# Performance work log

Hardware: AMD Instinct MI355X
Metric: run time of the kernel (lower is better)

Reference implementation:

```python
import jax, jax.numpy as jnp
import numpy as np
from jax import lax

B, N, S, K = 16, 8192, 1024, 32
FACTOR = 1.0
EPS_BN = 1e-5


def farthest_point_sample(xyz, npoint):
    # xyz: [B, N, 3] -> idx [B, npoint]. Deterministic start at index 0
    # (torch version starts at a random index; start choice doesn't change the math pattern).
    b, n, _ = xyz.shape
    bidx = jnp.arange(b)

    def step(carry, _):
        distance, farthest = carry
        centroid = xyz[bidx, farthest]                      # [B, 3]
        dist = jnp.sum((xyz - centroid[:, None, :]) ** 2, -1)  # [B, N]
        distance = jnp.minimum(distance, dist)
        new_far = jnp.argmax(distance, axis=-1)
        return (distance, new_far), farthest

    init = (jnp.full((b, n), 1e10, xyz.dtype), jnp.zeros((b,), jnp.int32))
    _, idxs = lax.scan(step, init, None, length=npoint)
    return idxs.T  # [B, npoint]


def square_distance(src, dst):
    # [B,Ns,3] x [B,Nd,3] -> [B,Ns,Nd]
    d = -2.0 * jnp.einsum('bnc,bmc->bnm', src, dst)
    d += jnp.sum(src ** 2, -1)[:, :, None]
    d += jnp.sum(dst ** 2, -1)[:, None, :]
    return d


def safe_cdist(x):
    # x: [B, C, S]; pairwise euclidean over rows -> [B, C, C]; zero-safe sqrt
    diff = x[:, :, None, :] - x[:, None, :, :]          # [B, C, C, S]
    sq = jnp.sum(diff * diff, -1)
    pos = sq > 0
    return jnp.where(pos, jnp.sqrt(jnp.where(pos, sq, 1.0)), 0.0)


def batchnorm(x, gamma, beta, axes):
    mean = jnp.mean(x, axes, keepdims=True)
    var = jnp.var(x, axes, keepdims=True)  # biased, as in torch BN normalization
    return (x - mean) / jnp.sqrt(var + EPS_BN) * gamma + beta


def reference(xyz, bn1_gamma, bn1_beta, bn2_gamma, bn2_beta):
    b = xyz.shape[0]
    # --- FPS sampling ---
    fps_idx = farthest_point_sample(lax.stop_gradient(xyz), S)          # [B,S]
    new_xyz = jnp.take_along_axis(xyz, fps_idx[:, :, None], axis=1)     # [B,S,3]
    # --- kNN grouping ---
    sq = square_distance(lax.stop_gradient(new_xyz), lax.stop_gradient(xyz))  # [B,S,N]
    _, knn_idx = lax.top_k(-sq, K)                                      # [B,S,K] indices
    grouped = jax.vmap(lambda p, i: p[i])(xyz, knn_idx)                 # [B,S,K,3]
    diff = grouped - new_xyz[:, :, None, :]
    std = jnp.std(diff, ddof=1)                                         # scalar, unbiased like torch.std
    knn_norm = diff / (std + 1e-5)
    center = jnp.broadcast_to(new_xyz[:, :, None, :], (b, S, K, 3))
    knn_xyz = jnp.concatenate([knn_norm, center], axis=-1)              # [B,S,K,6]
    # --- Pooling over neighbors ---
    x = jnp.transpose(knn_xyz, (0, 3, 1, 2))                            # [B,6,S,K]
    lc = jnp.max(x, -1) + jnp.mean(x, -1)                               # [B,6,S]
    lc = jax.nn.relu(batchnorm(lc, bn1_gamma[None, :, None], bn1_beta[None, :, None], (0, 2)))
    # --- Consecutive representation (cdist + superdiagonal factor) ---
    tfcw = safe_cdist(lc)                                               # [B,6,6]
    i = jnp.arange(5)
    tfcw = tfcw.at[:, i, i + 1].multiply(FACTOR)
    # --- Pooling2 ---
    feat = tfcw.reshape(b, -1)                                          # [B,36]
    feat = jax.nn.relu(batchnorm(feat, bn2_gamma[None, :], bn2_beta[None, :], (0,)))
    return feat


def setup_inputs() -> dict:
    key = jax.random.key(0)
    k1, = jax.random.split(key, 1)
    return {
        'xyz': jax.random.normal(k1, (B, N, 3), dtype=jnp.float32),
        'bn1_gamma': jnp.ones((6,), jnp.float32),
        'bn1_beta': jnp.zeros((6,), jnp.float32),
        'bn2_gamma': jnp.ones((36,), jnp.float32),
        'bn2_beta': jnp.zeros((36,), jnp.float32),
    }
```

## Files before the change

### kernel.cpp

```cpp
#include <hip/hip_runtime.h>
#include <hip/hip_bf16.h>

constexpr int BB = 16;
constexpr int NN = 8192;
constexpr int SS = 1024;
constexpr int KK = 32;
constexpr int BUFC = 256;

__device__ __forceinline__ float b2f(__hip_bfloat16 h) { return __bfloat162float(h); }

__device__ __forceinline__ unsigned mkey32(float d) {
    unsigned u = __float_as_uint(d);
    return u ^ (0x80000000u | (unsigned)((int)u >> 31));
}

__device__ __forceinline__ unsigned long long dist_key(const float* __restrict__ pb,
                                                       int idx, float qx, float qy,
                                                       float qz, float qq) {
    float px = pb[idx * 3 + 0];
    float py = pb[idx * 3 + 1];
    float pz = pb[idx * 3 + 2];
    float dot = __fadd_rn(__fadd_rn(__fmul_rn(qx, px), __fmul_rn(qy, py)), __fmul_rn(qz, pz));
    float pp  = __fadd_rn(__fadd_rn(__fmul_rn(px, px), __fmul_rn(py, py)), __fmul_rn(pz, pz));
    float d = __fadd_rn(__fadd_rn(__fmul_rn(-2.0f, dot), qq), pp);
    return ((unsigned long long)mkey32(d) << 32) | (unsigned)idx;
}

template <int CTRL, int RMASK>
__device__ __forceinline__ unsigned long long dppmove_u64(unsigned long long v) {
    int lo = (int)(unsigned)v, hi = (int)(unsigned)(v >> 32);
    int nlo = __builtin_amdgcn_update_dpp(lo, lo, CTRL, RMASK, 0xf, false);
    int nhi = __builtin_amdgcn_update_dpp(hi, hi, CTRL, RMASK, 0xf, false);
    return ((unsigned long long)(unsigned)nhi << 32) | (unsigned)nlo;
}

template <int CTRL, int RMASK>
__device__ __forceinline__ double dppmax_f64(double v) {
    double m = __longlong_as_double(
        dppmove_u64<CTRL, RMASK>((unsigned long long)__double_as_longlong(v)));
    return fmax(v, m);
}

__device__ __forceinline__ double wave_max_dpp_f64(double v) {
    v = dppmax_f64<0x121, 0xf>(v);
    v = dppmax_f64<0x122, 0xf>(v);
    v = dppmax_f64<0x124, 0xf>(v);
    v = dppmax_f64<0x128, 0xf>(v);
    v = dppmax_f64<0x142, 0xa>(v);
    v = dppmax_f64<0x143, 0xc>(v);
    return v;
}

__device__ __forceinline__ unsigned long long bitonic64(unsigned long long v, int lane) {
#pragma unroll
    for (int k = 2; k <= 64; k <<= 1) {
#pragma unroll
        for (int j = k >> 1; j > 0; j >>= 1) {
            unsigned long long p = __shfl_xor(v, j);
            bool up = ((lane & k) == 0);
            bool lower = ((lane & j) == 0);
            bool take_min = (up == lower);
            v = take_min ? (p < v ? p : v) : (p > v ? p : v);
        }
    }
    return v;
}

__device__ __forceinline__ unsigned expand3(unsigned v) {
    v &= 0x3FFu;
    v = (v | (v << 16)) & 0x030000FFu;
    v = (v | (v << 8))  & 0x0300F00Fu;
    v = (v | (v << 4))  & 0x030C30C3u;
    v = (v | (v << 2))  & 0x09249249u;
    return v;
}

__global__ __launch_bounds__(256) void convert_kernel(
    const void* __restrict__ xyz_raw, const void* __restrict__ g1r,
    const void* __restrict__ b1r, const void* __restrict__ g2r,
    const void* __restrict__ b2r, float* __restrict__ xyzf,
    float* __restrict__ params, void* __restrict__ out_raw) {
    const unsigned short* u = (const unsigned short*)xyz_raw;
    unsigned short s = u[2 * (threadIdx.x & 63)];
    int e = (s >> 7) & 0xFF;
    unsigned long long m = __ballot(e >= 100 && e <= 140);
    bool isbf = __popcll(m) > 48;

    const int NT = BB * NN * 3;
    int tid = blockIdx.x * blockDim.x + threadIdx.x;
    int stride = gridDim.x * blockDim.x;
    if (isbf) {
        const __hip_bfloat16* p = (const __hip_bfloat16*)xyz_raw;
        for (int i = tid; i < NT; i += stride) xyzf[i] = b2f(p[i]);
    } else {
        const float* p = (const float*)xyz_raw;
        for (int i = tid; i < NT; i += stride) xyzf[i] = p[i];
    }
    if (blockIdx.x == 0 && threadIdx.x < 85) {
        int t = threadIdx.x;
        if (t == 84) {
            params[84] = isbf ? 1.0f : 0.0f;
        } else {
            const void* src; int off;
            if (t < 6)       { src = g1r; off = t; }
            else if (t < 12) { src = b1r; off = t - 6; }
            else if (t < 48) { src = g2r; off = t - 12; }
            else             { src = b2r; off = t - 48; }
            params[t] = isbf ? b2f(((const __hip_bfloat16*)src)[off])
                             : ((const float*)src)[off];
        }
    }
    if (blockIdx.x == 1 && threadIdx.x < 64) {
        for (int i = threadIdx.x; i < 576; i += 64) {
            if (isbf) ((__hip_bfloat16*)out_raw)[i] = __float2bfloat16(1.0f);
            else      ((float*)out_raw)[i] = 1.0f;
        }
    }
}

__global__ __attribute__((amdgpu_flat_work_group_size(512, 512)))
__attribute__((amdgpu_waves_per_eu(2, 2)))
void fps_kernel(const float* __restrict__ xyzf, float* __restrict__ new_xyz) {
    constexpr int T = 512, P = NN / T;
    const int b = blockIdx.x, t = threadIdx.x;
    const float* xb = xyzf + (size_t)b * NN * 3;

    __shared__ float sxyz[NN * 3];
    __shared__ unsigned sortk[NN];
    __shared__ double skey[2][8];
    __shared__ float sred[6][8];
    __shared__ float sbb[6];

    for (int i = t; i < NN * 3; i += T) sxyz[i] = xb[i];
    __syncthreads();

    {
        float mn[3] = {3.4e38f, 3.4e38f, 3.4e38f};
        float mx[3] = {-3.4e38f, -3.4e38f, -3.4e38f};
        for (int j = 0; j < P; j++) {
            int p = t + j * T;
#pragma unroll
            for (int c = 0; c < 3; c++) {
                float v = sxyz[p * 3 + c];
                mn[c] = fminf(mn[c], v);
                mx[c] = fmaxf(mx[c], v);
            }
        }
#pragma unroll
        for (int o = 32; o > 0; o >>= 1) {
#pragma unroll
            for (int c = 0; c < 3; c++) {
                mn[c] = fminf(mn[c], __shfl_xor(mn[c], o));
                mx[c] = fmaxf(mx[c], __shfl_xor(mx[c], o));
            }
        }
        int wv = t >> 6, ln = t & 63;
        if (ln == 0) {
#pragma unroll
            for (int c = 0; c < 3; c++) { sred[c][wv] = mn[c]; sred[3 + c][wv] = mx[c]; }
        }
        __syncthreads();
        if (t < 6) {
            bool ismin = t < 3;
            float v = sred[t][0];
            for (int w = 1; w < 8; w++) v = ismin ? fminf(v, sred[t][w]) : fmaxf(v, sred[t][w]);
            sbb[t] = v;
        }
        __syncthreads();
    }

    {
        float bx = sbb[0], by = sbb[1], bz = sbb[2];
        float qsx = 63.0f / fmaxf(sbb[3] - bx, 1e-9f);
        float qsy = 63.0f / fmaxf(sbb[4] - by, 1e-9f);
        float qsz = 63.0f / fmaxf(sbb[5] - bz, 1e-9f);
        for (int p = t; p < NN; p += T) {
            unsigned qx = (unsigned)min(63, (int)((sxyz[p * 3 + 0] - bx) * qsx));
            unsigned qy = (unsigned)min(63, (int)((sxyz[p * 3 + 1] - by) * qsy));
            unsigned qz = (unsigned)min(63, (int)((sxyz[p * 3 + 2] - bz) * qsz));
            unsigned m = (expand3(qx) << 2) | (expand3(qy) << 1) | expand3(qz);
            sortk[p] = (m << 13) | (unsigned)p;
        }
        __syncthreads();
        for (unsigned k = 2; k <= (unsigned)NN; k <<= 1) {
            for (unsigned j = k >> 1; j > 0; j >>= 1) {
#pragma unroll
                for (int r = 0; r < NN / 2 / T; r++) {
                    unsigned gid = (unsigned)(r * T + t);
                    unsigned i = ((gid & ~(j - 1)) << 1) | (gid & (j - 1));
                    unsigned p2 = i | j;
                    unsigned a = sortk[i], c2 = sortk[p2];
                    bool up = ((i & k) == 0);
                    if ((a > c2) == up) { sortk[i] = c2; sortk[p2] = a; }
                }
                __syncthreads();
            }
        }
    }

    float px[P], py[P], pz[P], ds[P];
    int nidx[P];
    float lox = 3.4e38f, loy = 3.4e38f, loz = 3.4e38f;
    float hix = -3.4e38f, hiy = -3.4e38f, hiz = -3.4e38f;
#pragma unroll
    for (int j = 0; j < P; j++) {
        unsigned oi = sortk[t * P + j] & 8191u;
        float x = sxyz[oi * 3 + 0];
        float y = sxyz[oi * 3 + 1];
        float z = sxyz[oi * 3 + 2];
        px[j] = x; py[j] = y; pz[j] = z;
        ds[j] = 1e10f;
        nidx[j] = (int)~oi;
        lox = fminf(lox, x); hix = fmaxf(hix, x);
        loy = fminf(loy, y); hiy = fmaxf(hiy, y);
        loz = fminf(loz, z); hiz = fmaxf(hiz, z);
    }
    __syncthreads();
    float* samples = (float*)sortk;

    float cx = xb[0], cy = xb[1], cz = xb[2];
    if (t == 0) { samples[0] = cx; samples[1] = cy; samples[2] = cz; }
    const int wave = t >> 6, lane = t & 63;

    double bk = 0.0;
    float tb = 1e10f;

    for (int step = 1; step < SS; step++) {
        float ax = fmaxf(fmaxf(__fsub_rn(lox, cx), __fsub_rn(cx, hix)), 0.0f);
        float ay = fmaxf(fmaxf(__fsub_rn(loy, cy), __fsub_rn(cy, hiy)), 0.0f);
        float az = fmaxf(fmaxf(__fsub_rn(loz, cz), __fsub_rn(cz, hiz)), 0.0f);
        float lbd = ax * ax + ay * ay + az * az;
        if (lbd * 0.999f < tb) {
            double kk[P];
#pragma unroll
            for (int j = 0; j < P; j++) {
                float dx = __fsub_rn(px[j], cx);
                float dy = __fsub_rn(py[j], cy);
                float dz = __fsub_rn(pz[j], cz);
                float d = __fadd_rn(__fadd_rn(__fmul_rn(dx, dx), __fmul_rn(dy, dy)),
                                    __fmul_rn(dz, dz));
                float mm = fminf(ds[j], d);
                ds[j] = mm;
                kk[j] = __hiloint2double(__float_as_int(mm), nidx[j]);
            }
#pragma unroll
            for (int w2 = P / 2; w2 > 0; w2 >>= 1)
#pragma unroll
                for (int j = 0; j < w2; j++) kk[j] = fmax(kk[j], kk[j + w2]);
            bk = kk[0];
            tb = __uint_as_float((unsigned)__double2hiint(bk));
        }

        double wk = wave_max_dpp_f64(bk);
        const int par = step & 1;
        if (lane == 63) skey[par][wave] = wk;
        __syncthreads();

        double k0 = fmax(skey[par][0], skey[par][1]);
        double k1 = fmax(skey[par][2], skey[par][3]);
        double k2 = fmax(skey[par][4], skey[par][5]);
        double k3 = fmax(skey[par][6], skey[par][7]);
        double bkk = fmax(fmax(k0, k1), fmax(k2, k3));

        unsigned gidx = ~(unsigned)(unsigned long long)__double_as_longlong(bkk);
        cx = sxyz[gidx * 3 + 0];
        cy = sxyz[gidx * 3 + 1];
        cz = sxyz[gidx * 3 + 2];
        if (t == 0) {
            samples[step * 3 + 0] = cx;
            samples[step * 3 + 1] = cy;
            samples[step * 3 + 2] = cz;
        }
    }

    __syncthreads();
    float* o = new_xyz + (size_t)b * SS * 3;
    for (int i = t; i < SS * 3; i += T) o[i] = samples[i];
}

__global__ __launch_bounds__(256, 2) void knn_kernel(const float* __restrict__ xyzf,
                                                     const float* __restrict__ new_xyz,
                                                     float* __restrict__ A,
                                                     double* __restrict__ qstats) {
    __shared__ unsigned long long buf[4][BUFC];
    const int t = threadIdx.x;
    const int lane = t & 63, wv = t >> 6;
    const int w = blockIdx.x * 4 + wv;
    const int b = w >> 10, s = w & 1023;

    const float* q = new_xyz + ((size_t)b * SS + s) * 3;
    float qx = q[0], qy = q[1], qz = q[2];
    float qq = __fadd_rn(__fadd_rn(__fmul_rn(qx, qx), __fmul_rn(qy, qy)), __fmul_rn(qz, qz));

    const float* pb = xyzf + (size_t)b * NN * 3;
    const unsigned long long ltmask = (1ull << lane) - 1ull;

    unsigned long long lmin = ~0ull;
    for (int j = 0; j < 128; j++) {
        unsigned long long key = dist_key(pb, j * 64 + lane, qx, qy, qz, qq);
        lmin = key < lmin ? key : lmin;
    }

    unsigned long long vs = bitonic64(lmin, lane);
    unsigned long long That = __shfl(vs, 31);

    for (int i = lane; i < BUFC; i += 64) buf[wv][i] = ~0ull;
    int base = 0;
    for (int j = 0; j < 128; j++) {
        unsigned long long key = dist_key(pb, j * 64 + lane, qx, qy, qz, qq);
        bool f = key <= That;
        unsigned long long bal = __ballot(f);
        int pos = base + __popcll(bal & ltmask);
        if (f && pos < BUFC) buf[wv][pos] = key;
        base += __popcll(bal);
    }

    if (base > BUFC) {
        unsigned lo = 0, hi = (unsigned)(That >> 32);
        for (int it = 0; it < 32; it++) {
            unsigned mid = lo + ((hi - lo) >> 1);
            int c = 0;
            for (int j = 0; j < 128; j++) {
                unsigned long long key = dist_key(pb, j * 64 + lane, qx, qy, qz, qq);
                c += ((unsigned)(key >> 32) <= mid) ? 1 : 0;
            }
#pragma unroll
            for (int o = 32; o > 0; o >>= 1) c += __shfl_xor(c, o);
            if (c >= 32) hi = mid; else lo = mid + 1;
        }
        That = ((unsigned long long)hi << 32) | 0xFFFFFFFFull;
        for (int i = lane; i < BUFC; i += 64) buf[wv][i] = ~0ull;
        base = 0;
        for (int j = 0; j < 128; j++) {
            unsigned long long key = dist_key(pb, j * 64 + lane, qx, qy, qz, qq);
            bool f = key <= That;
            unsigned long long bal = __ballot(f);
            int pos = base + __popcll(bal & ltmask);
            if (f && pos < BUFC) buf[wv][pos] = key;
            base += __popcll(bal);
        }
        if (base > BUFC) base = BUFC;
    }

    int M = base;
    unsigned long long kept = ~0ull;
    if (M <= 64) {
        unsigned long long v = (lane < M) ? buf[wv][lane] : ~0ull;
        v = bitonic64(v, lane);
        kept = v;
    } else {
        unsigned long long c0 = buf[wv][lane];
        unsigned long long c1 = buf[wv][64 + lane];
        unsigned long long c2 = buf[wv][128 + lane];
        unsigned long long c3 = buf[wv][192 + lane];
        for (int r = 0; r < KK; r++) {
            unsigned long long m01 = c0 < c1 ? c0 : c1;
            unsigned long long m23 = c2 < c3 ? c2 : c3;
            unsigned long long mm = m01 < m23 ? m01 : m23;
#pragma unroll
            for (int o = 32; o > 0; o >>= 1) {
                unsigned long long t2 = __shfl_xor(mm, o);
                mm = t2 < mm ? t2 : mm;
            }
            if (lane == r) kept = mm;
            c0 = (c0 == mm) ? ~0ull : c0;
            c1 = (c1 == mm) ? ~0ull : c1;
            c2 = (c2 == mm) ? ~0ull : c2;
            c3 = (c3 == mm) ? ~0ull : c3;
        }
    }

    bool act = (lane < KK);
    float gx = 0.0f, gy = 0.0f, gz = 0.0f;
    if (act) {
        unsigned nidx = (unsigned)kept;
        gx = pb[nidx * 3 + 0];
        gy = pb[nidx * 3 + 1];
        gz = pb[nidx * 3 + 2];
    }
    float dx = __fsub_rn(gx, qx);
    float dy = __fsub_rn(gy, qy);
    float dz = __fsub_rn(gz, qz);
    float mx = act ? dx : -3.402823466e38f;
    float my = act ? dy : -3.402823466e38f;
    float mz = act ? dz : -3.402823466e38f;
    float sx = act ? dx : 0.0f;
    float sy = act ? dy : 0.0f;
    float sz = act ? dz : 0.0f;
    double s1 = act ? ((double)dx + (double)dy + (double)dz) : 0.0;
    double s2 = act ? ((double)dx * dx + (double)dy * dy + (double)dz * dz) : 0.0;
#pragma unroll
    for (int o = 32; o > 0; o >>= 1) {
        mx = fmaxf(mx, __shfl_xor(mx, o));
        my = fmaxf(my, __shfl_xor(my, o));
        mz = fmaxf(mz, __shfl_xor(mz, o));
        sx += __shfl_xor(sx, o);
        sy += __shfl_xor(sy, o);
        sz += __shfl_xor(sz, o);
        s1 += __shfl_xor(s1, o);
        s2 += __shfl_xor(s2, o);
    }
    if (lane == 0) {
        float* a = A + ((size_t)b * SS + s) * 3;
        a[0] = __fadd_rn(mx, __fmul_rn(sx, 0.03125f));
        a[1] = __fadd_rn(my, __fmul_rn(sy, 0.03125f));
        a[2] = __fadd_rn(mz, __fmul_rn(sz, 0.03125f));
        qstats[2 * w + 0] = s1;
        qstats[2 * w + 1] = s2;
    }
}

__global__ __launch_bounds__(256) void reduce_stats_kernel(const double* __restrict__ qstats,
                                                           double* __restrict__ stats) {
    __shared__ double r1[4], r2[4];
    int t = threadIdx.x;
    double a = 0.0, bsum = 0.0;
    for (int i = t; i < BB * SS; i += 256) { a += qstats[2 * i]; bsum += qstats[2 * i + 1]; }
#pragma unroll
    for (int o = 32; o > 0; o >>= 1) { a += __shfl_xor(a, o); bsum += __shfl_xor(bsum, o); }
    int wv = t >> 6, ln = t & 63;
    if (ln == 0) { r1[wv] = a; r2[wv] = bsum; }
    __syncthreads();
    if (t == 0) {
        stats[0] = r1[0] + r1[1] + r1[2] + r1[3];
        stats[1] = r2[0] + r2[1] + r2[2] + r2[3];
    }
}

__global__ __launch_bounds__(256) void lc_kernel(const float* __restrict__ new_xyz,
                                                 const float* __restrict__ A,
                                                 const double* __restrict__ stats,
                                                 float* __restrict__ lc,
                                                 double* __restrict__ bn1acc) {
    __shared__ double red[4];
    const int b = blockIdx.x / 6, c = blockIdx.x % 6;
    const int t = threadIdx.x;
    const double n = (double)BB * SS * KK * 3;
    double sd = stats[0], sq = stats[1];
    double var = (sq - sd * sd / n) / (n - 1.0);
    float stdv = (float)sqrt(var);
    float denom = __fadd_rn(stdv, 1e-5f);

    double s1 = 0.0, s2 = 0.0;
    for (int r = 0; r < 4; r++) {
        int s = r * 256 + t;
        float v;
        if (c < 3) {
            v = A[((size_t)b * SS + s) * 3 + c] / denom;
        } else {
            float ww = new_xyz[((size_t)b * SS + s) * 3 + (c - 3)];
            v = __fadd_rn(ww, ww);
        }
        lc[((size_t)b * 6 + c) * SS + s] = v;
        s1 += (double)v;
        s2 += (double)v * (double)v;
    }
#pragma unroll
    for (int off = 32; off > 0; off >>= 1) { s1 += __shfl_down(s1, off); s2 += __shfl_down(s2, off); }
    int wv = t >> 6, ln = t & 63;
    if (ln == 0) red[wv] = s1;
    __syncthreads();
    if (t == 0) atomicAdd(&bn1acc[c * 2 + 0], red[0] + red[1] + red[2] + red[3]);
    __syncthreads();
    if (ln == 0) red[wv] = s2;
    __syncthreads();
    if (t == 0) atomicAdd(&bn1acc[c * 2 + 1], red[0] + red[1] + red[2] + red[3]);
}

__global__ __launch_bounds__(256) void cdist_kernel(const float* __restrict__ lc,
                                                    const double* __restrict__ bn1acc,
                                                    const float* __restrict__ params,
                                                    float* __restrict__ tf) {
    __shared__ float sy[6 * SS];
    const int b = blockIdx.x, t = threadIdx.x;
    float mean[6], sde[6], gg[6], bt[6];
    const double n = (double)BB * SS;
#pragma unroll
    for (int c = 0; c < 6; c++) {
        double m = bn1acc[c * 2 + 0] / n;
        double v = bn1acc[c * 2 + 1] / n - m * m;
        mean[c] = (float)m;
        sde[c] = sqrtf((float)v + 1e-5f);
        gg[c] = params[c];
        bt[c] = params[6 + c];
    }
    for (int r = 0; r < 24; r++) {
        int g = r * 256 + t;
        int c = g >> 10;
        float v = lc[(size_t)b * 6 * SS + g];
        float y = (v - mean[c]) / sde[c] * gg[c] + bt[c];
        sy[g] = fmaxf(y, 0.0f);
    }
    __syncthreads();
    if (t < 6) tf[b * 36 + t * 7] = 0.0f;

    const int w = t >> 6, lane = t & 63;
    const int PI[15] = {0,0,0,0,0,1,1,1,1,2,2,2,3,3,4};
    const int PJ[15] = {1,2,3,4,5,2,3,4,5,3,4,5,4,5,5};
    for (int r = 0; r < 4; r++) {
        int p = w + r * 4;
        if (p < 15) {
            int i = PI[p], j = PJ[p];
            float acc = 0.0f;
            for (int m2 = 0; m2 < 16; m2++) {
                int s = lane + m2 * 64;
                float d = sy[i * SS + s] - sy[j * SS + s];
                acc += d * d;
            }
#pragma unroll
            for (int off = 32; off > 0; off >>= 1) acc += __shfl_down(acc, off);
            if (lane == 0) {
                float v = acc > 0.0f ? sqrtf(acc) : 0.0f;
                const float FACTOR = 1.0f;
                tf[b * 36 + i * 6 + j] = (j == i + 1) ? v * FACTOR : v;
                tf[b * 36 + j * 6 + i] = v;
            }
        }
    }
}

__global__ __launch_bounds__(64) void bn2_kernel(const float* __restrict__ tf,
                                                 const float* __restrict__ params,
                                                 void* __restrict__ out_raw) {
    int f = threadIdx.x;
    if (f >= 36) return;
    bool isbf = params[84] != 0.0f;
    float x[16]; float sum = 0.0f;
#pragma unroll
    for (int b = 0; b < 16; b++) { x[b] = tf[b * 36 + f]; sum += x[b]; }
    float mean = sum * 0.0625f;
    float vs = 0.0f;
#pragma unroll
    for (int b = 0; b < 16; b++) { float d = x[b] - mean; vs += d * d; }
    float var = vs * 0.0625f;
    float denom = sqrtf(var + 1e-5f);
    float g = params[12 + f], bb = params[48 + f];
#pragma unroll
    for (int b = 0; b < 16; b++) {
        float y = (x[b] - mean) / denom * g + bb;
        y = fmaxf(y, 0.0f);
        if (isbf) ((__hip_bfloat16*)out_raw)[b * 36 + f] = __float2bfloat16(y);
        else      ((float*)out_raw)[b * 36 + f] = y;
    }
}

extern "C" void kernel_launch(void* const* d_in, const int* in_sizes, int n_in,
                              void* d_out, int out_size, void* d_ws, size_t ws_size,
                              hipStream_t stream) {
    const void* xyz_raw = d_in[0];
    const void* g1r = d_in[1]; const void* b1r = d_in[2];
    const void* g2r = d_in[3]; const void* b2r = d_in[4];
    {
        const void* six[2] = {nullptr, nullptr}; int n6 = 0;
        const void* t36[2] = {nullptr, nullptr}; int n36 = 0;
        const void* big = nullptr;
        for (int i = 0; i < n_in; i++) {
            if (in_sizes[i] == BB * NN * 3) big = d_in[i];
            else if (in_sizes[i] == 6  && n6  < 2) six[n6++]  = d_in[i];
            else if (in_sizes[i] == 36 && n36 < 2) t36[n36++] = d_in[i];
        }
        if (big && n6 == 2 && n36 == 2) {
            xyz_raw = big; g1r = six[0]; b1r = six[1]; g2r = t36[0]; b2r = t36[1];
        }
    }

    char* ws = (char*)d_ws;
    float* xyzf    = (float*)(ws + 0);
    float* new_xyz = (float*)(ws + 1572864);
    float* A       = (float*)(ws + 1769472);
    float* lc      = (float*)(ws + 1966080);
    float* tf      = (float*)(ws + 2359296);
    double* stats  = (double*)(ws + 2361600);
    double* bn1acc = stats + 2;
    float* params  = (float*)(ws + 2361712);
    double* qstats = (double*)(ws + 2362112);

    hipMemsetAsync(stats, 0, 14 * sizeof(double), stream);
    hipLaunchKernelGGL(convert_kernel, dim3(512), dim3(256), 0, stream,
                       xyz_raw, g1r, b1r, g2r, b2r, xyzf, params, d_out);
    hipLaunchKernelGGL(fps_kernel,          dim3(16),   dim3(512), 0, stream, xyzf, new_xyz);
    hipLaunchKernelGGL(knn_kernel,          dim3(4096), dim3(256), 0, stream, xyzf, new_xyz, A, qstats);
    hipLaunchKernelGGL(reduce_stats_kernel, dim3(1),    dim3(256), 0, stream, qstats, stats);
    hipLaunchKernelGGL(lc_kernel,           dim3(96),   dim3(256), 0, stream, new_xyz, A, stats, lc, bn1acc);
    hipLaunchKernelGGL(cdist_kernel,        dim3(16),   dim3(256), 0, stream, lc, bn1acc, params, tf);
    hipLaunchKernelGGL(bn2_kernel,          dim3(1),    dim3(64),  0, stream, tf, params, d_out);

    (void)in_sizes; (void)n_in; (void)out_size; (void)ws_size;
}
```

Measured before the change: 1.155 ms.

## Process two batches per FPS block and carry winner coordinates through reduction

The FPS kernel now handles two batch elements per 512-thread block (8 blocks instead of 16). The two independent serial chains are interleaved within each step so their latencies overlap and share one barrier per step. The shared-memory copy of the point cloud is dropped; each wave picks out its winning point's coordinates from registers and publishes them alongside the key, so the cross-wave reduction yields the centroid directly. The wave reduction is now an all-lanes max using shuffles. In exchange, per-thread register pressure roughly doubles, which may cause spills, and only 8 CUs are used for this serial kernel.

```diff
diff --git a/kernel.cpp b/kernel.cpp
--- a/kernel.cpp
+++ b/kernel.cpp
@@ -41,13 +41,13 @@
     return fmax(v, m);
 }
 
-__device__ __forceinline__ double wave_max_dpp_f64(double v) {
+__device__ __forceinline__ double wave_allmax_f64(double v) {
     v = dppmax_f64<0x121, 0xf>(v);
     v = dppmax_f64<0x122, 0xf>(v);
     v = dppmax_f64<0x124, 0xf>(v);
     v = dppmax_f64<0x128, 0xf>(v);
-    v = dppmax_f64<0x142, 0xa>(v);
-    v = dppmax_f64<0x143, 0xc>(v);
+    v = fmax(v, __shfl_xor(v, 16));
+    v = fmax(v, __shfl_xor(v, 32));
     return v;
 }
 
@@ -73,6 +73,15 @@
     v = (v | (v << 4))  & 0x030C30C3u;
     v = (v | (v << 2))  & 0x09249249u;
     return v;
+}
+
+__device__ __forceinline__ void sel2(double& k, float& x, float& y, float& z,
+                                     double kb, float xb, float yb, float zb) {
+    bool g = kb > k;
+    k = g ? kb : k;
+    x = g ? xb : x;
+    y = g ? yb : y;
+    z = g ? zb : z;
 }
 
 __global__ __launch_bounds__(256) void convert_kernel(
@@ -123,159 +132,244 @@
 void fps_kernel(const float* __restrict__ xyzf, float* __restrict__ new_xyz) {
     constexpr int T = 512, P = NN / T;
     const int b = blockIdx.x, t = threadIdx.x;
-    const float* xb = xyzf + (size_t)b * NN * 3;
-
-    __shared__ float sxyz[NN * 3];
+    const float* xbA = xyzf + (size_t)(2 * b) * NN * 3;
+    const float* xbB = xyzf + (size_t)(2 * b + 1) * NN * 3;
+
     __shared__ unsigned sortk[NN];
-    __shared__ double skey[2][8];
+    __shared__ double skeyL[2][2][8];
+    __shared__ float4 scoordL[2][2][8];
     __shared__ float sred[6][8];
     __shared__ float sbb[6];
 
-    for (int i = t; i < NN * 3; i += T) sxyz[i] = xb[i];
+    const int wave = t >> 6, lane = t & 63;
+
+    float pxA[P], pyA[P], pzA[P], dsA[P]; unsigned uniA[P / 2];
+    float loxA, loyA, lozA, hixA, hiyA, hizA, cxA, cyA, czA;
+    float pxB[P], pyB[P], pzB[P], dsB[P]; unsigned uniB[P / 2];
+    float loxB, loyB, lozB, hixB, hiyB, hizB, cxB, cyB, czB;
+
+    auto setup = [&](const float* __restrict__ xb, float (&px)[P], float (&py)[P],
+                     float (&pz)[P], float (&ds)[P], unsigned (&uni)[P / 2],
+                     float& lox, float& loy, float& loz,
+                     float& hix, float& hiy, float& hiz,
+                     float& cx, float& cy, float& cz) {
+        {
+            float mn[3] = {3.4e38f, 3.4e38f, 3.4e38f};
+            float mx[3] = {-3.4e38f, -3.4e38f, -3.4e38f};
+            for (int j = 0; j < P; j++) {
+                int p = t + j * T;
+#pragma unroll
+                for (int c = 0; c < 3; c++) {
+                    float v = xb[p * 3 + c];
+                    mn[c] = fminf(mn[c], v);
+                    mx[c] = fmaxf(mx[c], v);
+                }
+            }
+#pragma unroll
+            for (int o = 32; o > 0; o >>= 1) {
+#pragma unroll
+                for (int c = 0; c < 3; c++) {
+                    mn[c] = fminf(mn[c], __shfl_xor(mn[c], o));
+                    mx[c] = fmaxf(mx[c], __shfl_xor(mx[c], o));
+                }
+            }
+            if (lane == 0) {
+#pragma unroll
+                for (int c = 0; c < 3; c++) { sred[c][wave] = mn[c]; sred[3 + c][wave] = mx[c]; }
+            }
+            __syncthreads();
+            if (t < 6) {
+                bool ismin = t < 3;
+                float v = sred[t][0];
+                for (int w = 1; w < 8; w++) v = ismin ? fminf(v, sred[t][w]) : fmaxf(v, sred[t][w]);
+                sbb[t] = v;
+            }
+            __syncthreads();
+        }
+        {
+            float bx = sbb[0], by = sbb[1], bz = sbb[2];
+            float qsx = 63.0f / fmaxf(sbb[3] - bx, 1e-9f);
+            float qsy = 63.0f / fmaxf(sbb[4] - by, 1e-9f);
+            float qsz = 63.0f / fmaxf(sbb[5] - bz, 1e-9f);
+            for (int p = t; p < NN; p += T) {
+                unsigned qx = (unsigned)min(63, (int)((xb[p * 3 + 0] - bx) * qsx));
+                unsigned qy = (unsigned)min(63, (int)((xb[p * 3 + 1] - by) * qsy));
+                unsigned qz = (unsigned)min(63, (int)((xb[p * 3 + 2] - bz) * qsz));
+                unsigned m = (expand3(qx) << 2) | (expand3(qy) << 1) | expand3(qz);
+                sortk[p] = (m << 13) | (unsigned)p;
+            }
+            __syncthreads();
+            for (unsigned k = 2; k <= (unsigned)NN; k <<= 1) {
+                for (unsigned j = k >> 1; j > 0; j >>= 1) {
+#pragma unroll
+                    for (int r = 0; r < NN / 2 / T; r++) {
+                        unsigned gid = (unsigned)(r * T + t);
+                        unsigned i = ((gid & ~(j - 1)) << 1) | (gid & (j - 1));
+                        unsigned p2 = i | j;
+                        unsigned a = sortk[i], c2 = sortk[p2];
+                        bool up = ((i & k) == 0);
+                        if ((a > c2) == up) { sortk[i] = c2; sortk[p2] = a; }
+                    }
+                    __syncthreads();
+                }
+            }
+        }
+        lox = 3.4e38f; loy = 3.4e38f; loz = 3.4e38f;
+        hix = -3.4e38f; hiy = -3.4e38f; hiz = -3.4e38f;
+#pragma unroll
+        for (int j = 0; j < P; j++) {
+            unsigned oi = sortk[t * P + j] & 8191u;
+            float x = xb[oi * 3 + 0];
+            float y = xb[oi * 3 + 1];
+            float z = xb[oi * 3 + 2];
+            px[j] = x; py[j] = y; pz[j] = z;
+            ds[j] = 1e10f;
+            if ((j & 1) == 0) uni[j >> 1] = oi; else uni[j >> 1] |= (oi << 16);
+            lox = fminf(lox, x); hix = fmaxf(hix, x);
+            loy = fminf(loy, y); hiy = fmaxf(hiy, y);
+            loz = fminf(loz, z); hiz = fmaxf(hiz, z);
+        }
+        cx = xb[0]; cy = xb[1]; cz = xb[2];
+        __syncthreads();
+    };
+
+    setup(xbA, pxA, pyA, pzA, dsA, uniA, loxA, loyA, lozA, hixA, hiyA, hizA, cxA, cyA, czA);
+    setup(xbB, pxB, pyB, pzB, dsB, uniB, loxB, loyB, lozB, hixB, hiyB, hizB, cxB, cyB, czB);
+
+    float* samplesA = (float*)sortk;
+    float* samplesB = samplesA + SS * 3;
+
+    if (t == 0) {
+        samplesA[0] = cxA; samplesA[1] = cyA; samplesA[2] = czA;
+        samplesB[0] = cxB; samplesB[1] = cyB; samplesB[2] = czB;
+    }
+
+    double bkA = 0.0, bkB = 0.0;
+    float tbA = 1e10f, tbB = 1e10f;
+
+    for (int step = 1; step < SS; step++) {
+        const int par = step & 1;
+
+        {
+            float ax = fmaxf(fmaxf(__fsub_rn(loxA, cxA), __fsub_rn(cxA, hixA)), 0.0f);
+            float ay = fmaxf(fmaxf(__fsub_rn(loyA, cyA), __fsub_rn(cyA, hiyA)), 0.0f);
+            float az = fmaxf(fmaxf(__fsub_rn(lozA, czA), __fsub_rn(czA, hizA)), 0.0f);
+            float lbd = ax * ax + ay * ay + az * az;
+            if (lbd * 0.999f < tbA) {
+                double kk[P];
+#pragma unroll
+                for (int j = 0; j < P; j++) {
+                    float dx = __fsub_rn(pxA[j], cxA);
+                    float dy = __fsub_rn(pyA[j], cyA);
+                    float dz = __fsub_rn(pzA[j], czA);
+                    float d = __fadd_rn(__fadd_rn(__fmul_rn(dx, dx), __fmul_rn(dy, dy)),
+                                        __fmul_rn(dz, dz));
+                    float mm = fminf(dsA[j], d);
+                    dsA[j] = mm;
+                    unsigned oi = (uniA[j >> 1] >> ((j & 1) * 16)) & 0xFFFFu;
+                    kk[j] = __hiloint2double(__float_as_int(mm), (int)~oi);
+                }
+#pragma unroll
+                for (int w2 = P / 2; w2 > 0; w2 >>= 1)
+#pragma unroll
+                    for (int j = 0; j < w2; j++) kk[j] = fmax(kk[j], kk[j + w2]);
+                bkA = kk[0];
+                tbA = __uint_as_float((unsigned)__double2hiint(bkA));
+            }
+            double wk = wave_allmax_f64(bkA);
+            if (bkA == wk) {
+                unsigned widx = ~(unsigned)(unsigned long long)__double_as_longlong(bkA);
+                float wx = pxA[0], wy = pyA[0], wz = pzA[0];
+#pragma unroll
+                for (int j = 1; j < P; j++) {
+                    unsigned oi = (uniA[j >> 1] >> ((j & 1) * 16)) & 0xFFFFu;
+                    bool m = (oi == widx);
+                    wx = m ? pxA[j] : wx; wy = m ? pyA[j] : wy; wz = m ? pzA[j] : wz;
+                }
+                skeyL[0][par][wave] = bkA;
+                scoordL[0][par][wave] = make_float4(wx, wy, wz, 0.0f);
+            }
+        }
+        {
+            float ax = fmaxf(fmaxf(__fsub_rn(loxB, cxB), __fsub_rn(cxB, hixB)), 0.0f);
+            float ay = fmaxf(fmaxf(__fsub_rn(loyB, cyB), __fsub_rn(cyB, hiyB)), 0.0f);
+            float az = fmaxf(fmaxf(__fsub_rn(lozB, czB), __fsub_rn(czB, hizB)), 0.0f);
+            float lbd = ax * ax + ay * ay + az * az;
+            if (lbd * 0.999f < tbB) {
+                double kk[P];
+#pragma unroll
+                for (int j = 0; j < P; j++) {
+                    float dx = __fsub_rn(pxB[j], cxB);
+                    float dy = __fsub_rn(pyB[j], cyB);
+                    float dz = __fsub_rn(pzB[j], czB);
+                    float d = __fadd_rn(__fadd_rn(__fmul_rn(dx, dx), __fmul_rn(dy, dy)),
+                                        __fmul_rn(dz, dz));
+                    float mm = fminf(dsB[j], d);
+                    dsB[j] = mm;
+                    unsigned oi = (uniB[j >> 1] >> ((j & 1) * 16)) & 0xFFFFu;
+                    kk[j] = __hiloint2double(__float_as_int(mm), (int)~oi);
+                }
+#pragma unroll
+                for (int w2 = P / 2; w2 > 0; w2 >>= 1)
+#pragma unroll
+                    for (int j = 0; j < w2; j++) kk[j] = fmax(kk[j], kk[j + w2]);
+                bkB = kk[0];
+                tbB = __uint_as_float((unsigned)__double2hiint(bkB));
+            }
+            double wk = wave_allmax_f64(bkB);
+            if (bkB == wk) {
+                unsigned widx = ~(unsigned)(unsigned long long)__double_as_longlong(bkB);
+                float wx = pxB[0], wy = pyB[0], wz = pzB[0];
+#pragma unroll
+                for (int j = 1; j < P; j++) {
+                    unsigned oi = (uniB[j >> 1] >> ((j & 1) * 16)) & 0xFFFFu;
+                    bool m = (oi == widx);
+                    wx = m ? pxB[j] : wx; wy = m ? pyB[j] : wy; wz = m ? pzB[j] : wz;
+                }
+                skeyL[1][par][wave] = bkB;
+                scoordL[1][par][wave] = make_float4(wx, wy, wz, 0.0f);
+            }
+        }
+
+        __syncthreads();
+
+        {
+            double K0 = skeyL[0][par][0], K1 = skeyL[0][par][1], K2 = skeyL[0][par][2], K3 = skeyL[0][par][3];
+            double K4 = skeyL[0][par][4], K5 = skeyL[0][par][5], K6 = skeyL[0][par][6], K7 = skeyL[0][par][7];
+            float4 C0 = scoordL[0][par][0], C1 = scoordL[0][par][1], C2 = scoordL[0][par][2], C3 = scoordL[0][par][3];
+            float4 C4 = scoordL[0][par][4], C5 = scoordL[0][par][5], C6 = scoordL[0][par][6], C7 = scoordL[0][par][7];
+            sel2(K0, C0.x, C0.y, C0.z, K1, C1.x, C1.y, C1.z);
+            sel2(K2, C2.x, C2.y, C2.z, K3, C3.x, C3.y, C3.z);
+            sel2(K4, C4.x, C4.y, C4.z, K5, C5.x, C5.y, C5.z);
+            sel2(K6, C6.x, C6.y, C6.z, K7, C7.x, C7.y, C7.z);
+            sel2(K0, C0.x, C0.y, C0.z, K2, C2.x, C2.y, C2.z);
+            sel2(K4, C4.x, C4.y, C4.z, K6, C6.x, C6.y, C6.z);
+            sel2(K0, C0.x, C0.y, C0.z, K4, C4.x, C4.y, C4.z);
+            cxA = C0.x; cyA = C0.y; czA = C0.z;
+        }
+        {
+            double K0 = skeyL[1][par][0], K1 = skeyL[1][par][1], K2 = skeyL[1][par][2], K3 = skeyL[1][par][3];
+            double K4 = skeyL[1][par][4], K5 = skeyL[1][par][5], K6 = skeyL[1][par][6], K7 = skeyL[1][par][7];
+            float4 C0 = scoordL[1][par][0], C1 = scoordL[1][par][1], C2 = scoordL[1][par][2], C3 = scoordL[1][par][3];
+            float4 C4 = scoordL[1][par][4], C5 = scoordL[1][par][5], C6 = scoordL[1][par][6], C7 = scoordL[1][par][7];
+            sel2(K0, C0.x, C0.y, C0.z, K1, C1.x, C1.y, C1.z);
+            sel2(K2, C2.x, C2.y, C2.z, K3, C3.x, C3.y, C3.z);
+            sel2(K4, C4.x, C4.y, C4.z, K5, C5.x, C5.y, C5.z);
+            sel2(K6, C6.x, C6.y, C6.z, K7, C7.x, C7.y, C7.z);
+            sel2(K0, C0.x, C0.y, C0.z, K2, C2.x, C2.y, C2.z);
+            sel2(K4, C4.x, C4.y, C4.z, K6, C6.x, C6.y, C6.z);
+            sel2(K0, C0.x, C0.y, C0.z, K4, C4.x, C4.y, C4.z);
+            cxB = C0.x; cyB = C0.y; czB = C0.z;
+        }
+        if (t == 0) {
+            samplesA[step * 3 + 0] = cxA; samplesA[step * 3 + 1] = cyA; samplesA[step * 3 + 2] = czA;
+            samplesB[step * 3 + 0] = cxB; samplesB[step * 3 + 1] = cyB; samplesB[step * 3 + 2] = czB;
+        }
+    }
+
     __syncthreads();
-
-    {
-        float mn[3] = {3.4e38f, 3.4e38f, 3.4e38f};
-        float mx[3] = {-3.4e38f, -3.4e38f, -3.4e38f};
-        for (int j = 0; j < P; j++) {
-            int p = t + j * T;
-#pragma unroll
-            for (int c = 0; c < 3; c++) {
-                float v = sxyz[p * 3 + c];
-                mn[c] = fminf(mn[c], v);
-                mx[c] = fmaxf(mx[c], v);
-            }
-        }
-#pragma unroll
-        for (int o = 32; o > 0; o >>= 1) {
-#pragma unroll
-            for (int c = 0; c < 3; c++) {
-                mn[c] = fminf(mn[c], __shfl_xor(mn[c], o));
-                mx[c] = fmaxf(mx[c], __shfl_xor(mx[c], o));
-            }
-        }
-        int wv = t >> 6, ln = t & 63;
-        if (ln == 0) {
-#pragma unroll
-            for (int c = 0; c < 3; c++) { sred[c][wv] = mn[c]; sred[3 + c][wv] = mx[c]; }
-        }
-        __syncthreads();
-        if (t < 6) {
-            bool ismin = t < 3;
-            float v = sred[t][0];
-            for (int w = 1; w < 8; w++) v = ismin ? fminf(v, sred[t][w]) : fmaxf(v, sred[t][w]);
-            sbb[t] = v;
-        }
-        __syncthreads();
-    }
-
-    {
-        float bx = sbb[0], by = sbb[1], bz = sbb[2];
-        float qsx = 63.0f / fmaxf(sbb[3] - bx, 1e-9f);
-        float qsy = 63.0f / fmaxf(sbb[4] - by, 1e-9f);
-        float qsz = 63.0f / fmaxf(sbb[5] - bz, 1e-9f);
-        for (int p = t; p < NN; p += T) {
-            unsigned qx = (unsigned)min(63, (int)((sxyz[p * 3 + 0] - bx) * qsx));
-            unsigned qy = (unsigned)min(63, (int)((sxyz[p * 3 + 1] - by) * qsy));
-            unsigned qz = (unsigned)min(63, (int)((sxyz[p * 3 + 2] - bz) * qsz));
-            unsigned m = (expand3(qx) << 2) | (expand3(qy) << 1) | expand3(qz);
-            sortk[p] = (m << 13) | (unsigned)p;
-        }
-        __syncthreads();
-        for (unsigned k = 2; k <= (unsigned)NN; k <<= 1) {
-            for (unsigned j = k >> 1; j > 0; j >>= 1) {
-#pragma unroll
-                for (int r = 0; r < NN / 2 / T; r++) {
-                    unsigned gid = (unsigned)(r * T + t);
-                    unsigned i = ((gid & ~(j - 1)) << 1) | (gid & (j - 1));
-                    unsigned p2 = i | j;
-                    unsigned a = sortk[i], c2 = sortk[p2];
-                    bool up = ((i & k) == 0);
-                    if ((a > c2) == up) { sortk[i] = c2; sortk[p2] = a; }
-                }
-                __syncthreads();
-            }
-        }
-    }
-
-    float px[P], py[P], pz[P], ds[P];
-    int nidx[P];
-    float lox = 3.4e38f, loy = 3.4e38f, loz = 3.4e38f;
-    float hix = -3.4e38f, hiy = -3.4e38f, hiz = -3.4e38f;
-#pragma unroll
-    for (int j = 0; j < P; j++) {
-        unsigned oi = sortk[t * P + j] & 8191u;
-        float x = sxyz[oi * 3 + 0];
-        float y = sxyz[oi * 3 + 1];
-        float z = sxyz[oi * 3 + 2];
-        px[j] = x; py[j] = y; pz[j] = z;
-        ds[j] = 1e10f;
-        nidx[j] = (int)~oi;
-        lox = fminf(lox, x); hix = fmaxf(hix, x);
-        loy = fminf(loy, y); hiy = fmaxf(hiy, y);
-        loz = fminf(loz, z); hiz = fmaxf(hiz, z);
-    }
-    __syncthreads();
-    float* samples = (float*)sortk;
-
-    float cx = xb[0], cy = xb[1], cz = xb[2];
-    if (t == 0) { samples[0] = cx; samples[1] = cy; samples[2] = cz; }
-    const int wave = t >> 6, lane = t & 63;
-
-    double bk = 0.0;
-    float tb = 1e10f;
-
-    for (int step = 1; step < SS; step++) {
-        float ax = fmaxf(fmaxf(__fsub_rn(lox, cx), __fsub_rn(cx, hix)), 0.0f);
-        float ay = fmaxf(fmaxf(__fsub_rn(loy, cy), __fsub_rn(cy, hiy)), 0.0f);
-        float az = fmaxf(fmaxf(__fsub_rn(loz, cz), __fsub_rn(cz, hiz)), 0.0f);
-        float lbd = ax * ax + ay * ay + az * az;
-        if (lbd * 0.999f < tb) {
-            double kk[P];
-#pragma unroll
-            for (int j = 0; j < P; j++) {
-                float dx = __fsub_rn(px[j], cx);
-                float dy = __fsub_rn(py[j], cy);
-                float dz = __fsub_rn(pz[j], cz);
-                float d = __fadd_rn(__fadd_rn(__fmul_rn(dx, dx), __fmul_rn(dy, dy)),
-                                    __fmul_rn(dz, dz));
-                float mm = fminf(ds[j], d);
-                ds[j] = mm;
-                kk[j] = __hiloint2double(__float_as_int(mm), nidx[j]);
-            }
-#pragma unroll
-            for (int w2 = P / 2; w2 > 0; w2 >>= 1)
-#pragma unroll
-                for (int j = 0; j < w2; j++) kk[j] = fmax(kk[j], kk[j + w2]);
-            bk = kk[0];
-            tb = __uint_as_float((unsigned)__double2hiint(bk));
-        }
-
-        double wk = wave_max_dpp_f64(bk);
-        const int par = step & 1;
-        if (lane == 63) skey[par][wave] = wk;
-        __syncthreads();
-
-        double k0 = fmax(skey[par][0], skey[par][1]);
-        double k1 = fmax(skey[par][2], skey[par][3]);
-        double k2 = fmax(skey[par][4], skey[par][5]);
-        double k3 = fmax(skey[par][6], skey[par][7]);
-        double bkk = fmax(fmax(k0, k1), fmax(k2, k3));
-
-        unsigned gidx = ~(unsigned)(unsigned long long)__double_as_longlong(bkk);
-        cx = sxyz[gidx * 3 + 0];
-        cy = sxyz[gidx * 3 + 1];
-        cz = sxyz[gidx * 3 + 2];
-        if (t == 0) {
-            samples[step * 3 + 0] = cx;
-            samples[step * 3 + 1] = cy;
-            samples[step * 3 + 2] = cz;
-        }
-    }
-
-    __syncthreads();
-    float* o = new_xyz + (size_t)b * SS * 3;
-    for (int i = t; i < SS * 3; i += T) o[i] = samples[i];
+    float* o = new_xyz + (size_t)(2 * b) * SS * 3;
+    for (int i = t; i < 2 * SS * 3; i += T) o[i] = samplesA[i];
 }
 
 __global__ __launch_bounds__(256, 2) void knn_kernel(const float* __restrict__ xyzf,
@@ -578,7 +672,7 @@
     hipMemsetAsync(stats, 0, 14 * sizeof(double), stream);
     hipLaunchKernelGGL(convert_kernel, dim3(512), dim3(256), 0, stream,
                        xyz_raw, g1r, b1r, g2r, b2r, xyzf, params, d_out);
-    hipLaunchKernelGGL(fps_kernel,          dim3(16),   dim3(512), 0, stream, xyzf, new_xyz);
+    hipLaunchKernelGGL(fps_kernel,          dim3(8),    dim3(512), 0, stream, xyzf, new_xyz);
     hipLaunchKernelGGL(knn_kernel,          dim3(4096), dim3(256), 0, stream, xyzf, new_xyz, A, qstats);
     hipLaunchKernelGGL(reduce_stats_kernel, dim3(1),    dim3(256), 0, stream, qstats, stats);
     hipLaunchKernelGGL(lc_kernel,           dim3(96),   dim3(256), 0, stream, new_xyz, A, stats, lc, bn1acc);
```

Result: slower. 2.852 ms (+147.0%).

## Pack two FPS batches per 1024-thread block and carry winner coords through reduction

Applied to the files above, without the earlier changes.

The FPS kernel now runs two batches in one 1024-thread workgroup (8 blocks instead of 16), each half keeping its own sort keys and sample buffers. The xyz copy in shared memory is dropped. Coordinates now come straight from global memory, and point indices are packed as 16-bit pairs to save registers. Each wave's winner writes its coordinates next to its key, so the per-step cross-wave reduction selects the centroid directly instead of doing a dependent shared-memory lookup. The risks are that only 8 CUs are busy, the block-wide barrier now couples two independent batches, and the higher waves-per-EU target puts pressure on registers.

```diff
diff --git a/kernel.cpp b/kernel.cpp
--- a/kernel.cpp
+++ b/kernel.cpp
@@ -41,13 +41,13 @@
     return fmax(v, m);
 }
 
-__device__ __forceinline__ double wave_max_dpp_f64(double v) {
+__device__ __forceinline__ double wave_allmax_f64(double v) {
     v = dppmax_f64<0x121, 0xf>(v);
     v = dppmax_f64<0x122, 0xf>(v);
     v = dppmax_f64<0x124, 0xf>(v);
     v = dppmax_f64<0x128, 0xf>(v);
-    v = dppmax_f64<0x142, 0xa>(v);
-    v = dppmax_f64<0x143, 0xc>(v);
+    v = fmax(v, __shfl_xor(v, 16));
+    v = fmax(v, __shfl_xor(v, 32));
     return v;
 }
 
@@ -73,6 +73,15 @@
     v = (v | (v << 4))  & 0x030C30C3u;
     v = (v | (v << 2))  & 0x09249249u;
     return v;
+}
+
+__device__ __forceinline__ void sel2(double& k, float& x, float& y, float& z,
+                                     double kb, float xb, float yb, float zb) {
+    bool g = kb > k;
+    k = g ? kb : k;
+    x = g ? xb : x;
+    y = g ? yb : y;
+    z = g ? zb : z;
 }
 
 __global__ __launch_bounds__(256) void convert_kernel(
@@ -118,30 +127,33 @@
     }
 }
 
-__global__ __attribute__((amdgpu_flat_work_group_size(512, 512)))
-__attribute__((amdgpu_waves_per_eu(2, 2)))
+__global__ __attribute__((amdgpu_flat_work_group_size(1024, 1024)))
+__attribute__((amdgpu_waves_per_eu(4, 4)))
 void fps_kernel(const float* __restrict__ xyzf, float* __restrict__ new_xyz) {
-    constexpr int T = 512, P = NN / T;
+    constexpr int T = 1024, HT = 512, P = NN / HT;
     const int b = blockIdx.x, t = threadIdx.x;
-    const float* xb = xyzf + (size_t)b * NN * 3;
-
-    __shared__ float sxyz[NN * 3];
-    __shared__ unsigned sortk[NN];
-    __shared__ double skey[2][8];
-    __shared__ float sred[6][8];
-    __shared__ float sbb[6];
-
-    for (int i = t; i < NN * 3; i += T) sxyz[i] = xb[i];
-    __syncthreads();
+    const int ht = t & 511;
+    const int bsel = t >> 9;
+    const float* xb = xyzf + (size_t)(2 * b + bsel) * NN * 3;
+
+    __shared__ unsigned sortkA[NN];
+    __shared__ unsigned sortkB[NN];
+    __shared__ double skey[2][2][8];
+    __shared__ float4 scoord[2][2][8];
+    __shared__ float sred[2][6][8];
+    __shared__ float sbb[2][6];
+
+    unsigned* myk = bsel ? sortkB : sortkA;
+    const int wave = t >> 6, lane = t & 63, hwave = wave & 7;
 
     {
         float mn[3] = {3.4e38f, 3.4e38f, 3.4e38f};
         float mx[3] = {-3.4e38f, -3.4e38f, -3.4e38f};
         for (int j = 0; j < P; j++) {
-            int p = t + j * T;
+            int p = ht + j * HT;
 #pragma unroll
             for (int c = 0; c < 3; c++) {
-                float v = sxyz[p * 3 + c];
+                float v = xb[p * 3 + c];
                 mn[c] = fminf(mn[c], v);
                 mx[c] = fmaxf(mx[c], v);
             }
@@ -154,44 +166,47 @@
                 mx[c] = fmaxf(mx[c], __shfl_xor(mx[c], o));
             }
         }
-        int wv = t >> 6, ln = t & 63;
-        if (ln == 0) {
-#pragma unroll
-            for (int c = 0; c < 3; c++) { sred[c][wv] = mn[c]; sred[3 + c][wv] = mx[c]; }
+        if (lane == 0) {
+#pragma unroll
+            for (int c = 0; c < 3; c++) {
+                sred[bsel][c][hwave] = mn[c];
+                sred[bsel][3 + c][hwave] = mx[c];
+            }
         }
         __syncthreads();
-        if (t < 6) {
-            bool ismin = t < 3;
-            float v = sred[t][0];
-            for (int w = 1; w < 8; w++) v = ismin ? fminf(v, sred[t][w]) : fmaxf(v, sred[t][w]);
-            sbb[t] = v;
+        if (ht < 6) {
+            bool ismin = ht < 3;
+            float v = sred[bsel][ht][0];
+            for (int w = 1; w < 8; w++)
+                v = ismin ? fminf(v, sred[bsel][ht][w]) : fmaxf(v, sred[bsel][ht][w]);
+            sbb[bsel][ht] = v;
         }
         __syncthreads();
     }
 
     {
-        float bx = sbb[0], by = sbb[1], bz = sbb[2];
-        float qsx = 63.0f / fmaxf(sbb[3] - bx, 1e-9f);
-        float qsy = 63.0f / fmaxf(sbb[4] - by, 1e-9f);
-        float qsz = 63.0f / fmaxf(sbb[5] - bz, 1e-9f);
-        for (int p = t; p < NN; p += T) {
-            unsigned qx = (unsigned)min(63, (int)((sxyz[p * 3 + 0] - bx) * qsx));
-            unsigned qy = (unsigned)min(63, (int)((sxyz[p * 3 + 1] - by) * qsy));
-            unsigned qz = (unsigned)min(63, (int)((sxyz[p * 3 + 2] - bz) * qsz));
+        float bx = sbb[bsel][0], by = sbb[bsel][1], bz = sbb[bsel][2];
+        float qsx = 63.0f / fmaxf(sbb[bsel][3] - bx, 1e-9f);
+        float qsy = 63.0f / fmaxf(sbb[bsel][4] - by, 1e-9f);
+        float qsz = 63.0f / fmaxf(sbb[bsel][5] - bz, 1e-9f);
+        for (int p = ht; p < NN; p += HT) {
+            unsigned qx = (unsigned)min(63, (int)((xb[p * 3 + 0] - bx) * qsx));
+            unsigned qy = (unsigned)min(63, (int)((xb[p * 3 + 1] - by) * qsy));
+            unsigned qz = (unsigned)min(63, (int)((xb[p * 3 + 2] - bz) * qsz));
             unsigned m = (expand3(qx) << 2) | (expand3(qy) << 1) | expand3(qz);
-            sortk[p] = (m << 13) | (unsigned)p;
+            myk[p] = (m << 13) | (unsigned)p;
         }
         __syncthreads();
         for (unsigned k = 2; k <= (unsigned)NN; k <<= 1) {
             for (unsigned j = k >> 1; j > 0; j >>= 1) {
 #pragma unroll
-                for (int r = 0; r < NN / 2 / T; r++) {
-                    unsigned gid = (unsigned)(r * T + t);
+                for (int r = 0; r < NN / 2 / HT; r++) {
+                    unsigned gid = (unsigned)(r * HT + ht);
                     unsigned i = ((gid & ~(j - 1)) << 1) | (gid & (j - 1));
                     unsigned p2 = i | j;
-                    unsigned a = sortk[i], c2 = sortk[p2];
+                    unsigned a = myk[i], c2 = myk[p2];
                     bool up = ((i & k) == 0);
-                    if ((a > c2) == up) { sortk[i] = c2; sortk[p2] = a; }
+                    if ((a > c2) == up) { myk[i] = c2; myk[p2] = a; }
                 }
                 __syncthreads();
             }
@@ -199,33 +214,37 @@
     }
 
     float px[P], py[P], pz[P], ds[P];
-    int nidx[P];
+    unsigned uni[P / 2];
     float lox = 3.4e38f, loy = 3.4e38f, loz = 3.4e38f;
     float hix = -3.4e38f, hiy = -3.4e38f, hiz = -3.4e38f;
 #pragma unroll
     for (int j = 0; j < P; j++) {
-        unsigned oi = sortk[t * P + j] & 8191u;
-        float x = sxyz[oi * 3 + 0];
-        float y = sxyz[oi * 3 + 1];
-        float z = sxyz[oi * 3 + 2];
+        unsigned oi = myk[ht * P + j] & 8191u;
+        float x = xb[oi * 3 + 0];
+        float y = xb[oi * 3 + 1];
+        float z = xb[oi * 3 + 2];
         px[j] = x; py[j] = y; pz[j] = z;
         ds[j] = 1e10f;
-        nidx[j] = (int)~oi;
+        if ((j & 1) == 0) uni[j >> 1] = oi; else uni[j >> 1] |= (oi << 16);
         lox = fminf(lox, x); hix = fmaxf(hix, x);
         loy = fminf(loy, y); hiy = fmaxf(hiy, y);
         loz = fminf(loz, z); hiz = fmaxf(hiz, z);
     }
     __syncthreads();
-    float* samples = (float*)sortk;
+
+    float* samplesA = (float*)sortkA;
+    float* samplesB = (float*)sortkB;
+    float* mysamples = bsel ? samplesB : samplesA;
 
     float cx = xb[0], cy = xb[1], cz = xb[2];
-    if (t == 0) { samples[0] = cx; samples[1] = cy; samples[2] = cz; }
-    const int wave = t >> 6, lane = t & 63;
+    if (ht == 0) { mysamples[0] = cx; mysamples[1] = cy; mysamples[2] = cz; }
 
     double bk = 0.0;
     float tb = 1e10f;
 
     for (int step = 1; step < SS; step++) {
+        const int par = step & 1;
+
         float ax = fmaxf(fmaxf(__fsub_rn(lox, cx), __fsub_rn(cx, hix)), 0.0f);
         float ay = fmaxf(fmaxf(__fsub_rn(loy, cy), __fsub_rn(cy, hiy)), 0.0f);
         float az = fmaxf(fmaxf(__fsub_rn(loz, cz), __fsub_rn(cz, hiz)), 0.0f);
@@ -241,7 +260,8 @@
                                     __fmul_rn(dz, dz));
                 float mm = fminf(ds[j], d);
                 ds[j] = mm;
-                kk[j] = __hiloint2double(__float_as_int(mm), nidx[j]);
+                unsigned oi = (uni[j >> 1] >> ((j & 1) * 16)) & 0xFFFFu;
+                kk[j] = __hiloint2double(__float_as_int(mm), (int)~oi);
             }
 #pragma unroll
             for (int w2 = P / 2; w2 > 0; w2 >>= 1)
@@ -251,31 +271,51 @@
             tb = __uint_as_float((unsigned)__double2hiint(bk));
         }
 
-        double wk = wave_max_dpp_f64(bk);
-        const int par = step & 1;
-        if (lane == 63) skey[par][wave] = wk;
+        double wk = wave_allmax_f64(bk);
+        if (bk == wk) {
+            unsigned widx = ~(unsigned)(unsigned long long)__double_as_longlong(bk);
+            float wx = px[0], wy = py[0], wz = pz[0];
+#pragma unroll
+            for (int j = 1; j < P; j++) {
+                unsigned oi = (uni[j >> 1] >> ((j & 1) * 16)) & 0xFFFFu;
+                bool m = (oi == widx);
+                wx = m ? px[j] : wx; wy = m ? py[j] : wy; wz = m ? pz[j] : wz;
+            }
+            skey[bsel][par][hwave] = bk;
+            scoord[bsel][par][hwave] = make_float4(wx, wy, wz, 0.0f);
+        }
+
         __syncthreads();
 
-        double k0 = fmax(skey[par][0], skey[par][1]);
-        double k1 = fmax(skey[par][2], skey[par][3]);
-        double k2 = fmax(skey[par][4], skey[par][5]);
-        double k3 = fmax(skey[par][6], skey[par][7]);
-        double bkk = fmax(fmax(k0, k1), fmax(k2, k3));
-
-        unsigned gidx = ~(unsigned)(unsigned long long)__double_as_longlong(bkk);
-        cx = sxyz[gidx * 3 + 0];
-        cy = sxyz[gidx * 3 + 1];
-        cz = sxyz[gidx * 3 + 2];
-        if (t == 0) {
-            samples[step * 3 + 0] = cx;
-            samples[step * 3 + 1] = cy;
-            samples[step * 3 + 2] = cz;
+        double K0 = skey[bsel][par][0], K1 = skey[bsel][par][1];
+        double K2 = skey[bsel][par][2], K3 = skey[bsel][par][3];
+        double K4 = skey[bsel][par][4], K5 = skey[bsel][par][5];
+        double K6 = skey[bsel][par][6], K7 = skey[bsel][par][7];
+        float4 C0 = scoord[bsel][par][0], C1 = scoord[bsel][par][1];
+        float4 C2 = scoord[bsel][par][2], C3 = scoord[bsel][par][3];
+        float4 C4 = scoord[bsel][par][4], C5 = scoord[bsel][par][5];
+        float4 C6 = scoord[bsel][par][6], C7 = scoord[bsel][par][7];
+        sel2(K0, C0.x, C0.y, C0.z, K1, C1.x, C1.y, C1.z);
+        sel2(K2, C2.x, C2.y, C2.z, K3, C3.x, C3.y, C3.z);
+        sel2(K4, C4.x, C4.y, C4.z, K5, C5.x, C5.y, C5.z);
+        sel2(K6, C6.x, C6.y, C6.z, K7, C7.x, C7.y, C7.z);
+        sel2(K0, C0.x, C0.y, C0.z, K2, C2.x, C2.y, C2.z);
+        sel2(K4, C4.x, C4.y, C4.z, K6, C6.x, C6.y, C6.z);
+        sel2(K0, C0.x, C0.y, C0.z, K4, C4.x, C4.y, C4.z);
+        cx = C0.x; cy = C0.y; cz = C0.z;
+        if (ht == 0) {
+            mysamples[step * 3 + 0] = cx;
+            mysamples[step * 3 + 1] = cy;
+            mysamples[step * 3 + 2] = cz;
         }
     }
 
     __syncthreads();
-    float* o = new_xyz + (size_t)b * SS * 3;
-    for (int i = t; i < SS * 3; i += T) o[i] = samples[i];
+    float* o = new_xyz + (size_t)(2 * b) * SS * 3;
+    for (int i = t; i < SS * 3; i += T) {
+        o[i] = samplesA[i];
+        o[SS * 3 + i] = samplesB[i];
+    }
 }
 
 __global__ __launch_bounds__(256, 2) void knn_kernel(const float* __restrict__ xyzf,
@@ -578,12 +618,12 @@
     hipMemsetAsync(stats, 0, 14 * sizeof(double), stream);
     hipLaunchKernelGGL(convert_kernel, dim3(512), dim3(256), 0, stream,
                        xyz_raw, g1r, b1r, g2r, b2r, xyzf, params, d_out);
-    hipLaunchKernelGGL(fps_kernel,          dim3(16),   dim3(512), 0, stream, xyzf, new_xyz);
-    hipLaunchKernelGGL(knn_kernel,          dim3(4096), dim3(256), 0, stream, xyzf, new_xyz, A, qstats);
-    hipLaunchKernelGGL(reduce_stats_kernel, dim3(1),    dim3(256), 0, stream, qstats, stats);
-    hipLaunchKernelGGL(lc_kernel,           dim3(96),   dim3(256), 0, stream, new_xyz, A, stats, lc, bn1acc);
-    hipLaunchKernelGGL(cdist_kernel,        dim3(16),   dim3(256), 0, stream, lc, bn1acc, params, tf);
-    hipLaunchKernelGGL(bn2_kernel,          dim3(1),    dim3(64),  0, stream, tf, params, d_out);
+    hipLaunchKernelGGL(fps_kernel,          dim3(8),    dim3(1024), 0, stream, xyzf, new_xyz);
+    hipLaunchKernelGGL(knn_kernel,          dim3(4096), dim3(256),  0, stream, xyzf, new_xyz, A, qstats);
+    hipLaunchKernelGGL(reduce_stats_kernel, dim3(1),    dim3(256),  0, stream, qstats, stats);
+    hipLaunchKernelGGL(lc_kernel,           dim3(96),   dim3(256),  0, stream, new_xyz, A, stats, lc, bn1acc);
+    hipLaunchKernelGGL(cdist_kernel,        dim3(16),   dim3(256),  0, stream, lc, bn1acc, params, tf);
+    hipLaunchKernelGGL(bn2_kernel,          dim3(1),    dim3(64),   0, stream, tf, params, d_out);
 
     (void)in_sizes; (void)n_in; (void)out_size; (void)ws_size;
 }
```

Measured after the change: 3.343 ms. 189% more time.
